# Kernel optimization log

Hardware: AMD Instinct MI355X
Metric: run time of the kernel (lower is better)

The kernel has to match this reference:

```python
import math
import jax, jax.numpy as jnp
import numpy as np

B, L, D, H = 4, 2048, 512, 8
DK = D // H  # d_keys = d_values = 64
KFAC = 3


def setup_inputs() -> dict:
    key = jax.random.key(0)
    ks = jax.random.split(key, 10)
    u_part = min(KFAC * int(math.ceil(math.log(L))), L)  # 24
    scale = 1.0 / math.sqrt(D)
    return {
        "queries": jax.random.normal(ks[0], (B, L, D), jnp.float32),
        "keys": jax.random.normal(ks[1], (B, L, D), jnp.float32),
        "values": jax.random.normal(ks[2], (B, L, D), jnp.float32),
        "index_sample": jax.random.randint(ks[3], (L, u_part), 0, L, jnp.int32),
        "Wq": jax.random.normal(ks[4], (D, D), jnp.float32) * scale,
        "bq": jnp.zeros((D,), jnp.float32),
        "Wk": jax.random.normal(ks[5], (D, D), jnp.float32) * scale,
        "bk": jnp.zeros((D,), jnp.float32),
        "Wv": jax.random.normal(ks[6], (D, D), jnp.float32) * scale,
        "bv": jnp.zeros((D,), jnp.float32),
        "Wo": jax.random.normal(ks[7], (D, D), jnp.float32) * scale,
        "bo": jnp.zeros((D,), jnp.float32),
    }


def reference(queries, keys, values, index_sample, Wq, bq, Wk, bk, Wv, bv, Wo, bo):
    b, q_len, d_out = queries.shape
    k_len = keys.shape[1]
    # projections -> [B, H, L, DK]
    q = (queries @ Wq + bq).reshape(b, q_len, H, DK).transpose(0, 2, 1, 3)
    k = (keys @ Wk + bk).reshape(b, k_len, H, DK).transpose(0, 2, 1, 3)
    v = (values @ Wv + bv).reshape(b, k_len, H, DK).transpose(0, 2, 1, 3)

    n_top = min(KFAC * int(math.ceil(math.log(q_len))), q_len)  # u

    # --- _prob_qk: sampled QK scores to pick sparse queries ---
    # k_sample: [B, H, q_len, sample_k, DK]
    k_sample = k[:, :, index_sample, :]
    q_k_sample = jnp.einsum("bhld,bhlsd->bhls", q, k_sample)
    m = jnp.max(q_k_sample, axis=-1) - jnp.sum(q_k_sample, axis=-1) / k_len
    _, m_top = jax.lax.top_k(m, n_top)  # [B, H, u]

    q_reduce = jnp.take_along_axis(q, m_top[..., None], axis=2)  # [B, H, u, DK]
    scores_top = jnp.einsum("bhud,bhkd->bhuk", q_reduce, k) / math.sqrt(d_out)

    # --- masked (causal) branch: mask_flag=True ---
    causal = jnp.triu(jnp.ones((q_len, k_len), bool), 1)
    indicator = causal[m_top]  # [B, H, u, k_len]
    scores_top = jnp.where(indicator, -jnp.inf, scores_top)

    attn = jax.nn.softmax(scores_top, axis=-1)  # [B, H, u, k_len]
    context = jnp.cumsum(v, axis=2)  # default context for non-selected queries
    attn_values = jnp.einsum("bhuk,bhkd->bhud", attn, v)

    bidx = jnp.arange(b)[:, None, None]
    hidx = jnp.arange(H)[None, :, None]
    context = context.at[bidx, hidx, m_top].set(attn_values)

    # mix=False: transpose back to [B, L, H, DV] then merge heads
    context = context.transpose(0, 2, 1, 3).reshape(b, q_len, H * DK)
    out = context @ Wo + bo  # dropout_rate=0 / inference: identity
    return out
```

## Files before the change

### kernel.cpp

```cpp
#include <hip/hip_runtime.h>
#include <hip/hip_bf16.h>
#include <math.h>

#define Bq 4
#define Lq 2048
#define Dq 512
#define Hq 8
#define DKq 64
#define Uq 24
#define TSCAN 16
#define NTILE (Lq / TSCAN)
#define NSUP 16
#define JCH 256
#define NCH (Lq / JCH)
#define TKCH 8

typedef unsigned short ushort_t;
typedef unsigned long long u64;
typedef __attribute__((ext_vector_type(8))) short bfrag8;
typedef __attribute__((ext_vector_type(4))) float facc4;

__device__ inline ushort_t bf16_rne(float f) {
  unsigned u = __float_as_uint(f);
  u += 0x7FFF + ((u >> 16) & 1);
  return (ushort_t)(u >> 16);
}
__device__ inline float bf16f(ushort_t h) {
  return __uint_as_float(((unsigned)h) << 16);
}
__device__ inline unsigned fkey(float f) {
  unsigned u = __float_as_uint(f);
  return (u & 0x80000000u) ? ~u : (u | 0x80000000u);
}
__device__ __forceinline__ void gl2lds16(const void* g, void* l) {
  __builtin_amdgcn_global_load_lds(
      (const __attribute__((address_space(1))) unsigned*)g,
      (__attribute__((address_space(3))) unsigned*)l, 16, 0, 0);
}

__global__ __launch_bounds__(256) void prep_all(
    const float* __restrict__ xq, const float* __restrict__ xk,
    const float* __restrict__ xv, ushort_t* __restrict__ qh,
    ushort_t* __restrict__ ql, ushort_t* __restrict__ kh,
    ushort_t* __restrict__ kl, ushort_t* __restrict__ vh,
    const float* __restrict__ W0, const float* __restrict__ W1,
    const float* __restrict__ W2, const float* __restrict__ W3,
    ushort_t* __restrict__ T0h, ushort_t* __restrict__ T0l,
    ushort_t* __restrict__ T1h, ushort_t* __restrict__ T1l,
    ushort_t* __restrict__ T2h, ushort_t* __restrict__ T3h) {
  __shared__ float tile[32][33];
  int y = blockIdx.y;
  if (y < 3) {
    const float* x = y == 0 ? xq : (y == 1 ? xk : xv);
    ushort_t* hi = y == 0 ? qh : (y == 1 ? kh : vh);
    ushort_t* lo = y == 0 ? ql : kl;
    int t = blockIdx.x * 256 + threadIdx.x;
    float4 v = *(const float4*)&x[(size_t)t * 4];
    ushort_t h0 = bf16_rne(v.x), h1 = bf16_rne(v.y), h2 = bf16_rne(v.z),
             h3 = bf16_rne(v.w);
    ushort4 hh = {h0, h1, h2, h3};
    *(ushort4*)&hi[(size_t)t * 4] = hh;
    if (y < 2) {
      ushort4 ll = {bf16_rne(v.x - bf16f(h0)), bf16_rne(v.y - bf16f(h1)),
                    bf16_rne(v.z - bf16f(h2)), bf16_rne(v.w - bf16f(h3))};
      *(ushort4*)&lo[(size_t)t * 4] = ll;
    }
    return;
  }
  int id = blockIdx.x;
  if (id >= 1024) return;
  int z = id >> 8;
  const float* W = z == 0 ? W0 : (z == 1 ? W1 : (z == 2 ? W2 : W3));
  ushort_t* Th = z == 0 ? T0h : (z == 1 ? T1h : (z == 2 ? T2h : T3h));
  ushort_t* Tl = z == 0 ? T0l : (z == 1 ? T1l : nullptr);
  int k0 = ((id >> 4) & 15) * 32, n0 = (id & 15) * 32;
  int tx = threadIdx.x & 31, ty = threadIdx.x >> 5;
  for (int r = ty; r < 32; r += 8)
    tile[tx][r] = W[(size_t)(k0 + r) * 512 + n0 + tx];
  __syncthreads();
  for (int r = ty; r < 32; r += 8) {
    float v = tile[r][tx];
    ushort_t h = bf16_rne(v);
    Th[(size_t)(n0 + r) * 512 + k0 + tx] = h;
    if (Tl) Tl[(size_t)(n0 + r) * 512 + k0 + tx] = bf16_rne(v - bf16f(h));
  }
}

__global__ __launch_bounds__(256) void gemm_qkv(
    const ushort_t* __restrict__ Aqh, const ushort_t* __restrict__ Aql,
    const ushort_t* __restrict__ Akh, const ushort_t* __restrict__ Akl,
    const ushort_t* __restrict__ Avh,
    const ushort_t* __restrict__ Wqh, const ushort_t* __restrict__ Wql,
    const ushort_t* __restrict__ Wkh, const ushort_t* __restrict__ Wkl,
    const ushort_t* __restrict__ Wvh,
    const float* __restrict__ bq, const float* __restrict__ bk,
    const float* __restrict__ bv,
    float* __restrict__ qo, float* __restrict__ ko, float* __restrict__ vo) {
  __shared__ ushort_t Ash[128][32], Asl[128][32];
  __shared__ ushort_t Bsh[128][32], Bsl[128][32];
  int which = blockIdx.z;
  const ushort_t* Ah = which == 0 ? Aqh : (which == 1 ? Akh : Avh);
  const ushort_t* Al = which == 0 ? Aql : Akl;
  const ushort_t* Bh = which == 0 ? Wqh : (which == 1 ? Wkh : Wvh);
  const ushort_t* Bl = which == 0 ? Wql : Wkl;
  const float* bias = which == 0 ? bq : (which == 1 ? bk : bv);
  float* C = which == 0 ? qo : (which == 1 ? ko : vo);
  const bool split = which < 2;

  int bm = blockIdx.x, bn = blockIdx.y;
  int tid = threadIdx.x;
  int wave = tid >> 6, lane = tid & 63;
  int wm = (wave & 1) * 64, wn = (wave >> 1) * 64;
  int quad = lane >> 4, lm = lane & 15;
  int srow = tid >> 2;
  int slc = (((tid & 3) ^ ((tid >> 3) & 3))) * 8;
  int sphys = (tid & 3) * 8;
  int rsw = (quad ^ ((lm >> 1) & 3)) * 8;
  facc4 acc[4][4] = {};

  for (int k0 = 0; k0 < 512; k0 += 32) {
#pragma unroll
    for (int p = 0; p < 2; ++p) {
      int row = srow + p * 64;
      size_t ga = (size_t)(bm * 128 + row) * 512 + k0 + slc;
      size_t gb = (size_t)(bn * 128 + row) * 512 + k0 + slc;
      gl2lds16(&Ah[ga], &Ash[row][sphys]);
      gl2lds16(&Bh[gb], &Bsh[row][sphys]);
      if (split) {
        gl2lds16(&Al[ga], &Asl[row][sphys]);
        gl2lds16(&Bl[gb], &Bsl[row][sphys]);
      }
    }
    __syncthreads();
    bfrag8 afh[4], afl[4], bfh[4], bfl[4];
#pragma unroll
    for (int mt = 0; mt < 4; ++mt) {
      afh[mt] = *(bfrag8*)&Ash[wm + mt * 16 + lm][rsw];
      if (split) afl[mt] = *(bfrag8*)&Asl[wm + mt * 16 + lm][rsw];
    }
#pragma unroll
    for (int nt = 0; nt < 4; ++nt) {
      bfh[nt] = *(bfrag8*)&Bsh[wn + nt * 16 + lm][rsw];
      if (split) bfl[nt] = *(bfrag8*)&Bsl[wn + nt * 16 + lm][rsw];
    }
#pragma unroll
    for (int mt = 0; mt < 4; ++mt)
#pragma unroll
      for (int nt = 0; nt < 4; ++nt) {
        facc4 a = acc[mt][nt];
        a = __builtin_amdgcn_mfma_f32_16x16x32_bf16(afh[mt], bfh[nt], a, 0, 0, 0);
        if (split) {
          a = __builtin_amdgcn_mfma_f32_16x16x32_bf16(afl[mt], bfh[nt], a, 0, 0, 0);
          a = __builtin_amdgcn_mfma_f32_16x16x32_bf16(afh[mt], bfl[nt], a, 0, 0, 0);
        }
        acc[mt][nt] = a;
      }
    __syncthreads();
  }
#pragma unroll
  for (int mt = 0; mt < 4; ++mt)
#pragma unroll
    for (int nt = 0; nt < 4; ++nt) {
      int col = bn * 128 + wn + nt * 16 + lm;
      float bv2 = bias[col];
#pragma unroll
      for (int r = 0; r < 4; ++r) {
        int row = bm * 128 + wm + mt * 16 + quad * 4 + r;
        C[(size_t)row * 512 + col] = acc[mt][nt][r] + bv2;
      }
    }
}

__global__ __launch_bounds__(256) void gemm_bf16(
    const ushort_t* __restrict__ A, const ushort_t* __restrict__ Bt,
    const float* __restrict__ bias, float* __restrict__ C) {
  __shared__ ushort_t As[128][32];
  __shared__ ushort_t Bs[128][32];
  int bm = blockIdx.x, bn = blockIdx.y;
  int tid = threadIdx.x;
  int wave = tid >> 6, lane = tid & 63;
  int wm = (wave & 1) * 64, wn = (wave >> 1) * 64;
  int quad = lane >> 4, lm = lane & 15;
  int srow = tid >> 2;
  int slc = (((tid & 3) ^ ((tid >> 3) & 3))) * 8;
  int sphys = (tid & 3) * 8;
  int rsw = (quad ^ ((lm >> 1) & 3)) * 8;
  facc4 acc[4][4] = {};

  for (int k0 = 0; k0 < 512; k0 += 32) {
#pragma unroll
    for (int p = 0; p < 2; ++p) {
      int row = srow + p * 64;
      gl2lds16(&A[(size_t)(bm * 128 + row) * 512 + k0 + slc], &As[row][sphys]);
      gl2lds16(&Bt[(size_t)(bn * 128 + row) * 512 + k0 + slc], &Bs[row][sphys]);
    }
    __syncthreads();
    bfrag8 af[4], bf[4];
#pragma unroll
    for (int mt = 0; mt < 4; ++mt)
      af[mt] = *(bfrag8*)&As[wm + mt * 16 + lm][rsw];
#pragma unroll
    for (int nt = 0; nt < 4; ++nt)
      bf[nt] = *(bfrag8*)&Bs[wn + nt * 16 + lm][rsw];
#pragma unroll
    for (int mt = 0; mt < 4; ++mt)
#pragma unroll
      for (int nt = 0; nt < 4; ++nt)
        acc[mt][nt] = __builtin_amdgcn_mfma_f32_16x16x32_bf16(
            af[mt], bf[nt], acc[mt][nt], 0, 0, 0);
    __syncthreads();
  }
#pragma unroll
  for (int mt = 0; mt < 4; ++mt)
#pragma unroll
    for (int nt = 0; nt < 4; ++nt) {
      int col = bn * 128 + wn + nt * 16 + lm;
      float bv = bias[col];
#pragma unroll
      for (int r = 0; r < 4; ++r) {
        int row = bm * 128 + wm + mt * 16 + quad * 4 + r;
        C[(size_t)row * 512 + col] = acc[mt][nt][r] + bv;
      }
    }
}

__global__ __launch_bounds__(256) void compute_m_tiles(
    const float* __restrict__ q, const float* __restrict__ k,
    const int* __restrict__ idxs, float* __restrict__ m,
    const float* __restrict__ v, float* __restrict__ tsum) {
  int bx = blockIdx.x;
  if (bx >= 4096) {
    int unit = (bx - 4096) * 2 + (threadIdx.x >> 7);
    int d4 = threadIdx.x & 127;
    int tile = unit & (NTILE - 1);
    int b = unit >> 7;
    float4 s = {0.f, 0.f, 0.f, 0.f};
    const float* base = &v[((size_t)b * Lq + tile * TSCAN) * Dq + d4 * 4];
#pragma unroll
    for (int r = 0; r < TSCAN; ++r) {
      float4 x = *(const float4*)&base[(size_t)r * Dq];
      s.x += x.x; s.y += x.y; s.z += x.z; s.w += x.w;
    }
    *(float4*)&tsum[((size_t)b * NTILE + tile) * Dq + d4 * 4] = s;
    return;
  }
  int wave = threadIdx.x >> 6, lane = threadIdx.x & 63;
  int lq = lane >> 4, dq = lane & 15;
  int slot = (bx * 4 + wave) * 4 + lq;
  int l = slot & (Lq - 1);
  int bh = slot >> 11;
  int h = bh & (Hq - 1), b = bh >> 3;
  float4 qv = *(const float4*)&q[((size_t)b * Lq + l) * Dq + h * DKq + dq * 4];
  const float* kb = &k[(size_t)b * Lq * Dq + h * DKq + dq * 4];
  const int* ib = &idxs[l * Uq];
  float mx = -INFINITY, sm = 0.f;
#pragma unroll
  for (int s = 0; s < Uq; ++s) {
    int j = ib[s];
    float4 kv = *(const float4*)&kb[(size_t)j * Dq];
    float p = qv.x * kv.x + qv.y * kv.y + qv.z * kv.z + qv.w * kv.w;
    p += __shfl_xor(p, 1, 64);
    p += __shfl_xor(p, 2, 64);
    p += __shfl_xor(p, 4, 64);
    p += __shfl_xor(p, 8, 64);
    mx = fmaxf(mx, p);
    sm += p;
  }
  if (dq == 0) m[slot] = mx - sm * (1.0f / Lq);
}

__global__ __launch_bounds__(256) void topk_stile(
    const float* __restrict__ m, int* __restrict__ mtop,
    int* __restrict__ repl, const float* __restrict__ tsum,
    float* __restrict__ stsum) {
  if (blockIdx.x >= 32) {
    int unit = (blockIdx.x - 32) * 2 + (threadIdx.x >> 7);
    int d4 = threadIdx.x & 127;
    int s = unit & (NSUP - 1);
    int b = unit >> 4;
    float4 acc = {0.f, 0.f, 0.f, 0.f};
    const float* tb = &tsum[((size_t)b * NTILE + s * 8) * Dq + d4 * 4];
#pragma unroll
    for (int i = 0; i < 8; ++i) {
      float4 t = *(const float4*)&tb[(size_t)i * Dq];
      acc.x += t.x; acc.y += t.y; acc.z += t.z; acc.w += t.w;
    }
    *(float4*)&stsum[((size_t)b * NSUP + s) * Dq + d4 * 4] = acc;
    return;
  }
  __shared__ u64 red[2][4];
  __shared__ int mt[Uq];
  int bh = blockIdx.x;
  int tid = threadIdx.x, wave = tid >> 6, lane = tid & 63;
  u64 keys[TKCH];
#pragma unroll
  for (int c = 0; c < TKCH; ++c) {
    int gidx = c * 256 + tid;
    float v = m[(size_t)bh * Lq + gidx];
    keys[c] = ((u64)fkey(v) << 32) | (u64)(Lq - 1 - gidx);
  }
#pragma unroll 1
  for (int it = 0; it < Uq; ++it) {
    u64 lb = keys[0];
#pragma unroll
    for (int c = 1; c < TKCH; ++c) lb = keys[c] > lb ? keys[c] : lb;
#pragma unroll
    for (int off = 32; off; off >>= 1) {
      u64 o = __shfl_xor(lb, off, 64);
      lb = o > lb ? o : lb;
    }
    int p = it & 1;
    if (lane == 0) red[p][wave] = lb;
    __syncthreads();
    u64 w0 = red[p][0] > red[p][1] ? red[p][0] : red[p][1];
    u64 w1 = red[p][2] > red[p][3] ? red[p][2] : red[p][3];
    u64 win = w0 > w1 ? w0 : w1;
    if (tid == 0) {
      int idx = Lq - 1 - (int)(win & 0xFFFFFFFFull);
      mtop[bh * Uq + it] = idx;
      mt[it] = idx;
    }
#pragma unroll
    for (int c = 0; c < TKCH; ++c)
      if (keys[c] == win) keys[c] = 0;
  }
  __syncthreads();
  int* rb = &repl[(size_t)bh * Lq];
#pragma unroll
  for (int c = 0; c < TKCH; ++c) rb[c * 256 + tid] = -1;
  __syncthreads();
  if (tid < Uq) rb[mt[tid]] = tid;
}

#define JT 256
#define JS 64

__global__ __launch_bounds__(256) void attn_fused(
    const float* __restrict__ q, const float* __restrict__ k,
    const float* __restrict__ v, const int* __restrict__ mtop,
    float* __restrict__ pmax, float* __restrict__ psum,
    float* __restrict__ pvp) {
  __shared__ float qs[Uq][DKq + 1];
  __shared__ float ks[JS][DKq + 1];
  __shared__ float es[Uq][260];
  __shared__ int i0s[Uq];
  int jt = blockIdx.x;
  int bh = blockIdx.y;
  int h = bh & (Hq - 1);
  int b = bh >> 3;
  int tid = threadIdx.x;
  if (tid < Uq) i0s[tid] = mtop[bh * Uq + tid];
  __syncthreads();
  int maxn = 0;
#pragma unroll
  for (int u2 = 0; u2 < Uq; ++u2) maxn = max(maxn, i0s[u2] + 1);
  int jbase0 = jt * JT;
  if (maxn <= jbase0) return;

  for (int s = tid; s < Uq * 16; s += 256) {
    int u = s >> 4, qd = (s & 15) * 4;
    float4 t = *(const float4*)&q[((size_t)b * Lq + i0s[u]) * Dq + h * DKq + qd];
    qs[u][qd] = t.x; qs[u][qd + 1] = t.y; qs[u][qd + 2] = t.z; qs[u][qd + 3] = t.w;
  }
  int jp = tid & 31;
  int ug = tid >> 5;
  float sreg[3][8] = {};
#pragma unroll
  for (int sub = 0; sub < 4; ++sub) {
    int jb = jbase0 + sub * JS;
    __syncthreads();
    if (jb < maxn) {
      for (int s = tid; s < JS * 16; s += 256) {
        int j = s >> 4, qd = (s & 15) * 4;
        float4 t =
            *(const float4*)&k[((size_t)b * Lq + jb + j) * Dq + h * DKq + qd];
        ks[j][qd] = t.x; ks[j][qd + 1] = t.y;
        ks[j][qd + 2] = t.z; ks[j][qd + 3] = t.w;
      }
    }
    __syncthreads();
    if (jb < maxn) {
      float acc[3][2] = {};
      int j0 = jp * 2, j1 = j0 + 1;
#pragma unroll 8
      for (int d = 0; d < DKq; ++d) {
        float k0 = ks[j0][d], k1 = ks[j1][d];
#pragma unroll
        for (int uu = 0; uu < 3; ++uu) {
          float qv = qs[ug * 3 + uu][d];
          acc[uu][0] += qv * k0;
          acc[uu][1] += qv * k1;
        }
      }
#pragma unroll
      for (int uu = 0; uu < 3; ++uu) {
        sreg[uu][sub * 2] = acc[uu][0];
        sreg[uu][sub * 2 + 1] = acc[uu][1];
      }
    }
  }

  const float scale = 0.044194173824159216f;
#pragma unroll
  for (int uu = 0; uu < 3; ++uu) {
    int u = ug * 3 + uu;
    int lu = i0s[u];
    float sv[8];
    float mx = -INFINITY;
#pragma unroll
    for (int t = 0; t < 8; ++t) {
      int jl = (t >> 1) * JS + jp * 2 + (t & 1);
      float x = sreg[uu][t] * scale;
      bool ok = (jbase0 + jl) <= lu;
      x = ok ? x : -INFINITY;
      sv[t] = x;
      mx = fmaxf(mx, x);
    }
#pragma unroll
    for (int off = 16; off; off >>= 1) mx = fmaxf(mx, __shfl_xor(mx, off, 64));
    float sm = 0.f;
#pragma unroll
    for (int t = 0; t < 8; ++t) {
      int jl = (t >> 1) * JS + jp * 2 + (t & 1);
      float e = (sv[t] == -INFINITY) ? 0.f : __expf(sv[t] - mx);
      es[u][jl] = e;
      sm += e;
    }
#pragma unroll
    for (int off = 16; off; off >>= 1) sm += __shfl_xor(sm, off, 64);
    if (jp == 0) {
      int blku = bh * Uq + u;
      pmax[blku * NCH + jt] = mx;
      psum[blku * NCH + jt] = sm;
    }
  }

  int wv = tid >> 6, lane = tid & 63;
  float a6[6] = {};
#pragma unroll
  for (int sub = 0; sub < 4; ++sub) {
    int jb = jbase0 + sub * JS;
    __syncthreads();
    if (jb < maxn) {
      for (int s = tid; s < JS * 16; s += 256) {
        int j = s >> 4, qd = (s & 15) * 4;
        float4 t =
            *(const float4*)&v[((size_t)b * Lq + jb + j) * Dq + h * DKq + qd];
        ks[j][qd] = t.x; ks[j][qd + 1] = t.y;
        ks[j][qd + 2] = t.z; ks[j][qd + 3] = t.w;
      }
    }
    __syncthreads();
    if (jb < maxn) {
#pragma unroll 4
      for (int j = 0; j < JS; j += 4) {
        float v0 = ks[j][lane], v1 = ks[j + 1][lane];
        float v2 = ks[j + 2][lane], v3 = ks[j + 3][lane];
#pragma unroll
        for (int uu = 0; uu < 6; ++uu) {
          float4 ee = *(const float4*)&es[wv * 6 + uu][sub * JS + j];
          a6[uu] += ee.x * v0 + ee.y * v1 + ee.z * v2 + ee.w * v3;
        }
      }
    }
  }
#pragma unroll
  for (int uu = 0; uu < 6; ++uu) {
    int blku = bh * Uq + wv * 6 + uu;
    pvp[((size_t)blku * NCH + jt) * DKq + lane] = a6[uu];
  }
}

__global__ __launch_bounds__(128) void build_context(
    const float* __restrict__ v, const float* __restrict__ tsum,
    const float* __restrict__ stsum, const int* __restrict__ repl,
    const float* __restrict__ pmax, const float* __restrict__ psum,
    const float* __restrict__ pvp, ushort_t* __restrict__ ctxh) {
  int blk = blockIdx.x;
  int tile = blk & (NTILE - 1);
  int b = blk >> 7;
  int d4 = threadIdx.x;
  int h = d4 >> 4;
  int sup = tile >> 3;
  float4 run = {0.f, 0.f, 0.f, 0.f};
  const float* sb = &stsum[(size_t)b * NSUP * Dq + d4 * 4];
  for (int s = 0; s < sup; ++s) {
    float4 t = *(const float4*)&sb[(size_t)s * Dq];
    run.x += t.x; run.y += t.y; run.z += t.z; run.w += t.w;
  }
  const float* tb = &tsum[((size_t)b * NTILE + sup * 8) * Dq + d4 * 4];
  int rem = tile & 7;
  for (int i = 0; i < rem; ++i) {
    float4 t = *(const float4*)&tb[(size_t)i * Dq];
    run.x += t.x; run.y += t.y; run.z += t.z; run.w += t.w;
  }
  const int* replb = &repl[(size_t)(b * Hq + h) * Lq + tile * TSCAN];
  const float* vb = &v[((size_t)b * Lq + tile * TSCAN) * Dq + d4 * 4];
  ushort_t* cb = &ctxh[((size_t)b * Lq + tile * TSCAN) * Dq + d4 * 4];
#pragma unroll
  for (int r = 0; r < TSCAN; ++r) {
    float4 x = *(const float4*)&vb[(size_t)r * Dq];
    run.x += x.x; run.y += x.y; run.z += x.z; run.w += x.w;
    int u = replb[r];
    float4 val = run;
    if (u >= 0) {
      int l = tile * TSCAN + r;
      int blku = (b * Hq + h) * Uq + u;
      int nc = (l + JCH) / JCH;
      float gmax = -INFINITY;
      for (int c = 0; c < nc; ++c) gmax = fmaxf(gmax, pmax[blku * NCH + c]);
      float tot = 0.f;
      float4 acc = {0.f, 0.f, 0.f, 0.f};
      for (int c = 0; c < nc; ++c) {
        float wgt = __expf(pmax[blku * NCH + c] - gmax);
        tot += psum[blku * NCH + c] * wgt;
        float4 pv = *(const float4*)&pvp[((size_t)blku * NCH + c) * DKq +
                                         (d4 & 15) * 4];
        acc.x += pv.x * wgt; acc.y += pv.y * wgt;
        acc.z += pv.z * wgt; acc.w += pv.w * wgt;
      }
      float inv = 1.0f / tot;
      val.x = acc.x * inv; val.y = acc.y * inv;
      val.z = acc.z * inv; val.w = acc.w * inv;
    }
    ushort4 o = {bf16_rne(val.x), bf16_rne(val.y), bf16_rne(val.z),
                 bf16_rne(val.w)};
    *(ushort4*)&cb[(size_t)r * Dq] = o;
  }
}

extern "C" void kernel_launch(void* const* d_in, const int* in_sizes, int n_in,
                              void* d_out, int out_size, void* d_ws,
                              size_t ws_size, hipStream_t stream) {
  const float* queries = (const float*)d_in[0];
  const float* keys    = (const float*)d_in[1];
  const float* values  = (const float*)d_in[2];
  const int*   idxs    = (const int*)d_in[3];
  const float* Wq = (const float*)d_in[4];
  const float* bq = (const float*)d_in[5];
  const float* Wk = (const float*)d_in[6];
  const float* bk = (const float*)d_in[7];
  const float* Wv = (const float*)d_in[8];
  const float* bv = (const float*)d_in[9];
  const float* Wo = (const float*)d_in[10];
  const float* bo = (const float*)d_in[11];
  float* out = (float*)d_out;

  const size_t BLD = (size_t)Bq * Lq * Dq;
  char* w = (char*)d_ws;
  float* q    = (float*)w; w += BLD * 4;
  float* k    = (float*)w; w += BLD * 4;
  float* v    = (float*)w; w += BLD * 4;
  float* m    = (float*)w; w += (size_t)Bq * Hq * Lq * 4;
  float* tsum = (float*)w; w += (size_t)Bq * NTILE * Dq * 4;
  float* stsum= (float*)w; w += (size_t)Bq * NSUP * Dq * 4;
  int* mtop   = (int*)w;   w += Bq * Hq * Uq * 4;
  int* repl   = (int*)w;   w += (size_t)Bq * Hq * Lq * 4;
  float* pmax = (float*)w; w += (size_t)Bq * Hq * Uq * NCH * 4;
  float* psum = (float*)w; w += (size_t)Bq * Hq * Uq * NCH * 4;
  float* pvp  = (float*)w; w += (size_t)Bq * Hq * Uq * NCH * DKq * 4;
  ushort_t* ctxh = (ushort_t*)w; w += BLD * 2;
  ushort_t* Aqh = (ushort_t*)w; w += BLD * 2;
  ushort_t* Aql = (ushort_t*)w; w += BLD * 2;
  ushort_t* Akh = (ushort_t*)w; w += BLD * 2;
  ushort_t* Akl = (ushort_t*)w; w += BLD * 2;
  ushort_t* Avh = (ushort_t*)w; w += BLD * 2;
  const size_t WSZ = 512 * 512;
  ushort_t* Wqh = (ushort_t*)w; w += WSZ * 2;
  ushort_t* Wql = (ushort_t*)w; w += WSZ * 2;
  ushort_t* Wkh = (ushort_t*)w; w += WSZ * 2;
  ushort_t* Wkl = (ushort_t*)w; w += WSZ * 2;
  ushort_t* Wvh = (ushort_t*)w; w += WSZ * 2;
  ushort_t* Woh = (ushort_t*)w; w += WSZ * 2;

  {
    dim3 pgrid(BLD / 4 / 256, 4);
    prep_all<<<pgrid, 256, 0, stream>>>(queries, keys, values, Aqh, Aql, Akh,
                                        Akl, Avh, Wq, Wk, Wv, Wo, Wqh, Wql,
                                        Wkh, Wkl, Wvh, Woh);
  }

  {
    dim3 ggrid(64, 4, 3);
    gemm_qkv<<<ggrid, 256, 0, stream>>>(Aqh, Aql, Akh, Akl, Avh, Wqh, Wql,
                                        Wkh, Wkl, Wvh, bq, bk, bv, q, k, v);
  }

  compute_m_tiles<<<4096 + 256, 256, 0, stream>>>(q, k, idxs, m, v, tsum);

  topk_stile<<<64, 256, 0, stream>>>(m, mtop, repl, tsum, stsum);

  {
    dim3 agrid(Lq / JT, Bq * Hq);
    attn_fused<<<agrid, 256, 0, stream>>>(q, k, v, mtop, pmax, psum, pvp);
  }

  build_context<<<Bq * NTILE, 128, 0, stream>>>(v, tsum, stsum, repl, pmax,
                                                psum, pvp, ctxh);

  {
    dim3 ggrid(64, 4);
    gemm_bf16<<<ggrid, 256, 0, stream>>>(ctxh, Woh, bo, out);
  }
}
```

Before: 258.5 us.

## Fuse V tile sums into QKV GEMM epilogue and halve attention key chunks

The per-16-row column sums of V, which feed the cumulative-sum context, are now computed inside the V GEMM epilogue from the accumulators using cross-quad shuffles. This removes the extra blocks that re-read V from global memory in the m-computation kernel. Separately, the attention chunk width is cut from 256 to 128 keys, doubling the grid and the partial softmax entries for better occupancy and finer causal skipping. The cost is more partial results to merge and a slightly longer GEMM epilogue.

```diff
diff --git a/kernel.cpp b/kernel.cpp
--- a/kernel.cpp
+++ b/kernel.cpp
@@ -11,7 +11,7 @@
 #define TSCAN 16
 #define NTILE (Lq / TSCAN)
 #define NSUP 16
-#define JCH 256
+#define JCH 128
 #define NCH (Lq / JCH)
 #define TKCH 8
 
@@ -95,7 +95,8 @@
     const ushort_t* __restrict__ Wvh,
     const float* __restrict__ bq, const float* __restrict__ bk,
     const float* __restrict__ bv,
-    float* __restrict__ qo, float* __restrict__ ko, float* __restrict__ vo) {
+    float* __restrict__ qo, float* __restrict__ ko, float* __restrict__ vo,
+    float* __restrict__ tsum) {
   __shared__ ushort_t Ash[128][32], Asl[128][32];
   __shared__ ushort_t Bsh[128][32], Bsl[128][32];
   int which = blockIdx.z;
@@ -169,6 +170,26 @@
         C[(size_t)row * 512 + col] = acc[mt][nt][r] + bv2;
       }
     }
+  if (which == 2) {
+#pragma unroll
+    for (int mt = 0; mt < 4; ++mt) {
+      int rowbase = bm * 128 + wm + mt * 16;
+      int vb2 = rowbase >> 11;
+      int ltile = (rowbase & (Lq - 1)) >> 4;
+#pragma unroll
+      for (int nt = 0; nt < 4; ++nt) {
+        float s = acc[mt][nt][0] + acc[mt][nt][1] + acc[mt][nt][2] +
+                  acc[mt][nt][3];
+        s += __shfl_xor(s, 16, 64);
+        s += __shfl_xor(s, 32, 64);
+        if (quad == 0) {
+          int col = bn * 128 + wn + nt * 16 + lm;
+          tsum[((size_t)vb2 * NTILE + ltile) * Dq + col] =
+              s + 16.0f * bias[col];
+        }
+      }
+    }
+  }
 }
 
 __global__ __launch_bounds__(256) void gemm_bf16(
@@ -224,29 +245,12 @@
     }
 }
 
-__global__ __launch_bounds__(256) void compute_m_tiles(
+__global__ __launch_bounds__(256) void compute_m(
     const float* __restrict__ q, const float* __restrict__ k,
-    const int* __restrict__ idxs, float* __restrict__ m,
-    const float* __restrict__ v, float* __restrict__ tsum) {
-  int bx = blockIdx.x;
-  if (bx >= 4096) {
-    int unit = (bx - 4096) * 2 + (threadIdx.x >> 7);
-    int d4 = threadIdx.x & 127;
-    int tile = unit & (NTILE - 1);
-    int b = unit >> 7;
-    float4 s = {0.f, 0.f, 0.f, 0.f};
-    const float* base = &v[((size_t)b * Lq + tile * TSCAN) * Dq + d4 * 4];
-#pragma unroll
-    for (int r = 0; r < TSCAN; ++r) {
-      float4 x = *(const float4*)&base[(size_t)r * Dq];
-      s.x += x.x; s.y += x.y; s.z += x.z; s.w += x.w;
-    }
-    *(float4*)&tsum[((size_t)b * NTILE + tile) * Dq + d4 * 4] = s;
-    return;
-  }
+    const int* __restrict__ idxs, float* __restrict__ m) {
   int wave = threadIdx.x >> 6, lane = threadIdx.x & 63;
   int lq = lane >> 4, dq = lane & 15;
-  int slot = (bx * 4 + wave) * 4 + lq;
+  int slot = (blockIdx.x * 4 + wave) * 4 + lq;
   int l = slot & (Lq - 1);
   int bh = slot >> 11;
   int h = bh & (Hq - 1), b = bh >> 3;
@@ -332,7 +336,6 @@
   if (tid < Uq) rb[mt[tid]] = tid;
 }
 
-#define JT 256
 #define JS 64
 
 __global__ __launch_bounds__(256) void attn_fused(
@@ -342,7 +345,7 @@
     float* __restrict__ pvp) {
   __shared__ float qs[Uq][DKq + 1];
   __shared__ float ks[JS][DKq + 1];
-  __shared__ float es[Uq][260];
+  __shared__ float es[Uq][132];
   __shared__ int i0s[Uq];
   int jt = blockIdx.x;
   int bh = blockIdx.y;
@@ -354,7 +357,7 @@
   int maxn = 0;
 #pragma unroll
   for (int u2 = 0; u2 < Uq; ++u2) maxn = max(maxn, i0s[u2] + 1);
-  int jbase0 = jt * JT;
+  int jbase0 = jt * JCH;
   if (maxn <= jbase0) return;
 
   for (int s = tid; s < Uq * 16; s += 256) {
@@ -364,9 +367,9 @@
   }
   int jp = tid & 31;
   int ug = tid >> 5;
-  float sreg[3][8] = {};
-#pragma unroll
-  for (int sub = 0; sub < 4; ++sub) {
+  float sreg[3][4] = {};
+#pragma unroll
+  for (int sub = 0; sub < 2; ++sub) {
     int jb = jbase0 + sub * JS;
     __syncthreads();
     if (jb < maxn) {
@@ -405,10 +408,10 @@
   for (int uu = 0; uu < 3; ++uu) {
     int u = ug * 3 + uu;
     int lu = i0s[u];
-    float sv[8];
+    float sv[4];
     float mx = -INFINITY;
 #pragma unroll
-    for (int t = 0; t < 8; ++t) {
+    for (int t = 0; t < 4; ++t) {
       int jl = (t >> 1) * JS + jp * 2 + (t & 1);
       float x = sreg[uu][t] * scale;
       bool ok = (jbase0 + jl) <= lu;
@@ -420,7 +423,7 @@
     for (int off = 16; off; off >>= 1) mx = fmaxf(mx, __shfl_xor(mx, off, 64));
     float sm = 0.f;
 #pragma unroll
-    for (int t = 0; t < 8; ++t) {
+    for (int t = 0; t < 4; ++t) {
       int jl = (t >> 1) * JS + jp * 2 + (t & 1);
       float e = (sv[t] == -INFINITY) ? 0.f : __expf(sv[t] - mx);
       es[u][jl] = e;
@@ -438,7 +441,7 @@
   int wv = tid >> 6, lane = tid & 63;
   float a6[6] = {};
 #pragma unroll
-  for (int sub = 0; sub < 4; ++sub) {
+  for (int sub = 0; sub < 2; ++sub) {
     int jb = jbase0 + sub * JS;
     __syncthreads();
     if (jb < maxn) {
@@ -583,15 +586,16 @@
   {
     dim3 ggrid(64, 4, 3);
     gemm_qkv<<<ggrid, 256, 0, stream>>>(Aqh, Aql, Akh, Akl, Avh, Wqh, Wql,
-                                        Wkh, Wkl, Wvh, bq, bk, bv, q, k, v);
-  }
-
-  compute_m_tiles<<<4096 + 256, 256, 0, stream>>>(q, k, idxs, m, v, tsum);
+                                        Wkh, Wkl, Wvh, bq, bk, bv, q, k, v,
+                                        tsum);
+  }
+
+  compute_m<<<(Bq * Hq * Lq) / 16, 256, 0, stream>>>(q, k, idxs, m);
 
   topk_stile<<<64, 256, 0, stream>>>(m, mtop, repl, tsum, stsum);
 
   {
-    dim3 agrid(Lq / JT, Bq * Hq);
+    dim3 agrid(Lq / JCH, Bq * Hq);
     attn_fused<<<agrid, 256, 0, stream>>>(q, k, v, mtop, pmax, psum, pvp);
   }
 
```

Result: slower. 289.1 us (+11.9%).
